# Kernel tuning notes

Hardware: AMD Instinct MI355X
Metric: run time of the kernel (lower is better)

Reference implementation:

```python
import jax, jax.numpy as jnp
import numpy as np

EPS = 1e-5
DIL = 1
PAD = 1
STRIDE = 1

def conv2d(x, w, stride=1, pad=1, dil=1):
    return jax.lax.conv_general_dilated(x, w, (stride, stride), [(pad, pad), (pad, pad)],
                                        rhs_dilation=(dil, dil),
                                        dimension_numbers=('NCHW', 'OIHW', 'NCHW'))

def batchnorm(x, g, b, m, v):
    inv = g / jnp.sqrt(v + EPS)
    return x * inv[None, :, None, None] + (b - m * inv)[None, :, None, None]

def _bilinear(img, y, x):
    # img: [C,H,W]; y,x: [Ho,Wo] float sample coords; zero padding outside.
    H, W = img.shape[1], img.shape[2]
    y0 = jnp.floor(y); x0 = jnp.floor(x)
    ty = y - y0; tx = x - x0
    y0i = y0.astype(jnp.int32); x0i = x0.astype(jnp.int32)
    def g(yi, xi):
        valid = (yi >= 0) & (yi < H) & (xi >= 0) & (xi < W)
        v = img[:, jnp.clip(yi, 0, H - 1), jnp.clip(xi, 0, W - 1)]  # [C,Ho,Wo]
        return jnp.where(valid[None], v, jnp.zeros((), img.dtype))
    return (g(y0i, x0i) * ((1 - ty) * (1 - tx))[None]
            + g(y0i, x0i + 1) * ((1 - ty) * tx)[None]
            + g(y0i + 1, x0i) * (ty * (1 - tx))[None]
            + g(y0i + 1, x0i + 1) * (ty * tx)[None])

def deform_conv(x, w, offset, stride=1, pad=1, dil=1):
    # offset: [B, 18, Ho, Wo], channels 0:9 = dy per kernel tap (row-major), 9:18 = dx.
    B, C, H, W = x.shape
    Co = w.shape[0]
    Ho = (H + 2 * pad - dil * 2 - 1) // stride + 1
    Wo = (W + 2 * pad - dil * 2 - 1) // stride + 1
    off = offset.reshape(B, 2, 9, Ho, Wo)
    iy = (jnp.arange(Ho) * stride - pad).astype(x.dtype)
    ix = (jnp.arange(Wo) * stride - pad).astype(x.dtype)
    wk = w.reshape(Co, C, 9)
    out = jnp.zeros((B, Co, Ho, Wo), x.dtype)
    for k in range(9):  # fixed 3x3 kernel taps
        ky, kx = k // 3, k % 3
        ys = iy[:, None] + ky * dil + off[:, 0, k]  # [B,Ho,Wo]
        xs = ix[None, :] + kx * dil + off[:, 1, k]
        val = jax.vmap(_bilinear)(x, ys, xs)        # [B,C,Ho,Wo]
        out = out + jnp.einsum('bchw,oc->bohw', val, wk[:, :, k])
    return out

def offset_bias(dil, dtype):
    bw = jnp.array([[-1., 0., 1.]] * 3, dtype) * (dil - 1)
    bh = bw.T
    return jnp.concatenate([bh.reshape(-1), bw.reshape(-1)])  # [18]

def setup_inputs() -> dict:
    key = jax.random.key(0)
    ks = jax.random.split(key, 12)
    B, C, H, W = 8, 256, 56, 56
    inp = {
        'x': jax.random.normal(ks[0], (B, C, H, W), jnp.float32),
        'conv1_w': jax.random.normal(ks[1], (C, C, 3, 3), jnp.float32) * 0.02,
        'bn1_g': jax.random.normal(ks[2], (C,), jnp.float32) * 0.1 + 1.0,
        'bn1_b': jax.random.normal(ks[3], (C,), jnp.float32) * 0.1,
        'bn1_m': jax.random.normal(ks[4], (C,), jnp.float32) * 0.1,
        'bn1_v': jax.random.uniform(ks[5], (C,), jnp.float32) + 0.5,
        'off_w': jax.random.normal(ks[6], (18, C, 3, 3), jnp.float32) * 0.01,
        'off_b': jnp.zeros((18,), jnp.float32),
        'conv2_w': jax.random.normal(ks[7], (C, C, 3, 3), jnp.float32) * 0.02,
        'bn2_g': jax.random.normal(ks[8], (C,), jnp.float32) * 0.1 + 1.0,
        'bn2_b': jax.random.normal(ks[9], (C,), jnp.float32) * 0.1,
        'bn2_m': jax.random.normal(ks[10], (C,), jnp.float32) * 0.1,
        'bn2_v': jax.random.uniform(ks[11], (C,), jnp.float32) + 0.5,
    }
    return inp

def reference(x, conv1_w, bn1_g, bn1_b, bn1_m, bn1_v, off_w, off_b, conv2_w, bn2_g, bn2_b, bn2_m, bn2_v):
    residual = x
    out = conv2d(x, conv1_w, STRIDE, PAD, DIL)
    out = jax.nn.relu(batchnorm(out, bn1_g, bn1_b, bn1_m, bn1_v))
    offset = conv2d(out, off_w, STRIDE, PAD, DIL) + off_b[None, :, None, None]
    offset = offset + offset_bias(DIL, out.dtype)[None, :, None, None]
    out = deform_conv(out, conv2_w, offset, STRIDE, PAD, DIL)
    out = batchnorm(out, bn2_g, bn2_b, bn2_m, bn2_v)
    return jax.nn.relu(out + residual)
```

## Files before the change

kernel.cpp:

```cpp
#include <hip/hip_runtime.h>

#define NB 8
#define NH 56
#define NW 56
#define NHW 3136
#define NCHW 802816
#define NPIX 25088
#define NHP 58
#define EPSV 1e-5f

typedef float f32x4 __attribute__((ext_vector_type(4)));
typedef __bf16 bf16x8 __attribute__((ext_vector_type(8)));

__device__ __forceinline__ unsigned short f2b(float f) {
  unsigned int u = __float_as_uint(f);
  u += 0x7FFFu + ((u >> 16) & 1u);
  return (unsigned short)(u >> 16);
}
__device__ __forceinline__ float blo(unsigned int u){ return __uint_as_float(u << 16); }
__device__ __forceinline__ float bhi(unsigned int u){ return __uint_as_float(u & 0xFFFF0000u); }
__device__ __forceinline__ unsigned int pack_trunc(float f0, float f1) {
  return __builtin_amdgcn_perm(__float_as_uint(f1), __float_as_uint(f0), 0x07060302u);
}
__device__ __forceinline__ void soft_barrier() {
  __builtin_amdgcn_s_waitcnt(0xC07F);
  __builtin_amdgcn_s_barrier();
}

__global__ __launch_bounds__(256) void clear_borders(
    unsigned short* __restrict__ xbp, unsigned short* __restrict__ t1b)
{
  int i = blockIdx.x*256 + threadIdx.x;
  int q = i & 31; int pid = i >> 5;
  int b = pid / 228, j = pid % 228;
  int y, x;
  if (j < 58)       { y = 0;  x = j; }
  else if (j < 116) { y = 57; x = j - 58; }
  else { int jj = j - 116; y = 1 + (jj >> 1); x = (jj & 1) * 57; }
  size_t addr = ((size_t)(b*NHP + y)*NHP + x)*256 + q*8;
  uint4 z = make_uint4(0u,0u,0u,0u);
  *(uint4*)(xbp + addr) = z;
  *(uint4*)(t1b + addr) = z;
}

__global__ __launch_bounds__(256) void prep_x(
    const float* __restrict__ x, unsigned short* __restrict__ xbp)
{
  __shared__ float T[64][65];
  const int pxt  = blockIdx.x * 64;
  const int cg   = blockIdx.y * 64;
  const int b    = pxt / NHW;
  const int rem0 = pxt % NHW;
  const int t    = threadIdx.x;
  const int pl   = t & 63;
  const int c0   = t >> 6;
  const float* src = x + (size_t)b*NCHW + rem0;
  #pragma unroll
  for (int it = 0; it < 16; ++it) {
    int c = c0 + it*4;
    T[c][pl] = src[(size_t)(cg + c)*NHW + pl];
  }
  __syncthreads();
  const int pr = t >> 5;
  const int cp = t & 31;
  #pragma unroll
  for (int it = 0; it < 8; ++it) {
    int pxl = pr + it*8;
    int rem = rem0 + pxl;
    int ho = rem / NW, wo = rem % NW;
    unsigned int pk = ((unsigned int)f2b(T[cp*2+1][pxl]) << 16) | (unsigned int)f2b(T[cp*2][pxl]);
    *(unsigned int*)(xbp + ((size_t)(b*NHP + ho + 1)*NHP + (wo + 1))*256 + cg + cp*2) = pk;
  }
}

__global__ __launch_bounds__(256) void prep_w(
    const float* __restrict__ w, unsigned short* __restrict__ wp)
{
  int i = blockIdx.x*256 + threadIdx.x;
  int co = i / 2304;
  int r  = i % 2304;
  int k  = r >> 8;
  int ci = r & 255;
  wp[i] = f2b(w[((size_t)co*256 + ci)*9 + k]);
}

__global__ __launch_bounds__(256) void prep_w3(
    const float* __restrict__ ow, unsigned short* __restrict__ w3p)
{
  int i = blockIdx.x*256 + threadIdx.x;
  int co = i / 2304;
  int r  = i % 2304;
  int k  = r >> 8;
  int ci = r & 255;
  w3p[i] = (co < 18) ? f2b(ow[((size_t)co*256 + ci)*9 + k]) : (unsigned short)0;
}

__global__ __launch_bounds__(512, 4) void gemm_conv1(
    const unsigned short* __restrict__ xbp, const unsigned short* __restrict__ w1p,
    const float* __restrict__ gam, const float* __restrict__ bet,
    const float* __restrict__ mu,  const float* __restrict__ var,
    unsigned short* __restrict__ t1b)
{
  __shared__ unsigned short SMEM[20480];
  unsigned short* Al = SMEM;
  unsigned short* Bl = SMEM + 4096;

  const int m0   = blockIdx.x * 64;
  const int t    = threadIdx.x;
  const int lane = t & 63;
  const int wv   = t >> 6;
  const int wvM  = wv & 1;
  const int wvN  = wv >> 1;
  const int quad = lane >> 4;
  const int l15  = lane & 15;

  const int srow = t >> 3;
  const int seg  = t & 7;
  const int sxor = srow & 7;
  const int px  = m0 + srow;
  const int b   = px / NHW, rem = px % NHW;
  const int ho  = rem / NW, wo = rem % NW;
  const unsigned int pbase = ((unsigned int)(b*NHP + ho)*NHP + wo)*256u + seg*8u;

  f32x4 acc[2][4];
  #pragma unroll
  for (int i = 0; i < 2; ++i)
    #pragma unroll
    for (int j = 0; j < 4; ++j) acc[i][j] = (f32x4)(0.f);

  uint4 pA, pB0, pB1, pB2, pB3;
  {
    pA  = *(const uint4*)(xbp + pbase);
    const unsigned int rb = seg*8u;
    pB0 = *(const uint4*)(w1p + (size_t)(srow      )*2304 + rb);
    pB1 = *(const uint4*)(w1p + (size_t)(srow +  64)*2304 + rb);
    pB2 = *(const uint4*)(w1p + (size_t)(srow + 128)*2304 + rb);
    pB3 = *(const uint4*)(w1p + (size_t)(srow + 192)*2304 + rb);
  }

  for (int r = 0; r < 36; ++r) {
    __syncthreads();
    *(uint4*)(&Al[srow*64 + ((seg ^ sxor)*8)]) = pA;
    *(uint4*)(&Bl[(srow      )*64 + ((seg ^ sxor)*8)]) = pB0;
    *(uint4*)(&Bl[(srow +  64)*64 + ((seg ^ sxor)*8)]) = pB1;
    *(uint4*)(&Bl[(srow + 128)*64 + ((seg ^ sxor)*8)]) = pB2;
    *(uint4*)(&Bl[(srow + 192)*64 + ((seg ^ sxor)*8)]) = pB3;
    {
      const int rn = (r < 35) ? r + 1 : 35;
      const int kn = rn >> 2, cicn = rn & 3;
      const int kyn = kn/3, kxn = kn - kyn*3;
      pA  = *(const uint4*)(xbp + pbase + (unsigned int)((kyn*NHP + kxn)*256 + cicn*64));
      const unsigned int rb = (unsigned int)(rn*64) + seg*8u;
      pB0 = *(const uint4*)(w1p + (size_t)(srow      )*2304 + rb);
      pB1 = *(const uint4*)(w1p + (size_t)(srow +  64)*2304 + rb);
      pB2 = *(const uint4*)(w1p + (size_t)(srow + 128)*2304 + rb);
      pB3 = *(const uint4*)(w1p + (size_t)(srow + 192)*2304 + rb);
    }
    soft_barrier();
    #pragma unroll
    for (int kk = 0; kk < 2; ++kk) {
      const int s8 = (kk*4 + quad) ^ (l15 & 7);
      bf16x8 af[2], bfr[4];
      #pragma unroll
      for (int mt = 0; mt < 2; ++mt)
        af[mt] = *(const bf16x8*)(&Al[(wvM*32 + mt*16 + l15)*64 + s8*8]);
      #pragma unroll
      for (int nt = 0; nt < 4; ++nt)
        bfr[nt] = *(const bf16x8*)(&Bl[(wvN*64 + nt*16 + l15)*64 + s8*8]);
      #pragma unroll
      for (int mt = 0; mt < 2; ++mt)
        #pragma unroll
        for (int nt = 0; nt < 4; ++nt)
          acc[mt][nt] = __builtin_amdgcn_mfma_f32_16x16x32_bf16(af[mt], bfr[nt], acc[mt][nt], 0, 0, 0);
    }
  }

  __syncthreads();
  unsigned short* Sw = SMEM + wv*2304;
  #pragma unroll
  for (int nt = 0; nt < 4; ++nt) {
    const int co = wvN*64 + nt*16 + l15;
    const float inv  = gam[co] * rsqrtf(var[co] + EPSV);
    const float beta = bet[co] - mu[co]*inv;
    #pragma unroll
    for (int mt = 0; mt < 2; ++mt) {
      #pragma unroll
      for (int rr = 0; rr < 4; ++rr) {
        const int pxl = mt*16 + quad*4 + rr;
        float val = acc[mt][nt][rr]*inv + beta;
        val = val > 0.f ? val : 0.f;
        Sw[pxl*72 + nt*16 + l15] = f2b(val);
      }
    }
  }
  #pragma unroll
  for (int i = 0; i < 4; ++i) {
    const int pxl = (lane >> 3) + 8*i;
    const int sc  = lane & 7;
    uint4 q = *(const uint4*)(&Sw[pxl*72 + sc*8]);
    const int pg = m0 + wvM*32 + pxl;
    const int bb = pg / NHW, rm = pg % NHW;
    const int hh = rm / NW, ww = rm % NW;
    *(uint4*)(t1b + ((size_t)(bb*NHP + hh + 1)*NHP + ww + 1)*256 + wvN*64 + sc*8) = q;
  }
}

__global__ __launch_bounds__(256, 8) void gemm_off(
    const unsigned short* __restrict__ t1b, const unsigned short* __restrict__ w3p,
    const float* __restrict__ ob, float* __restrict__ toff)
{
  __shared__ unsigned short Al[4096];
  __shared__ unsigned short Bl[2048];

  const int m0 = blockIdx.x * 64;
  const int kc = blockIdx.y;
  const int t    = threadIdx.x;
  const int lane = t & 63;
  const int wv   = t >> 6;
  const int quad = lane >> 4;
  const int l15  = lane & 15;

  const int arow = t >> 2;
  const int as4  = t & 3;
  const int axor = arow & 7;
  const int pxa  = m0 + arow;
  const int ba   = pxa / NHW, rema = pxa % NHW;
  const unsigned int pbase = ((unsigned int)(ba*NHP + rema/NW)*NHP + rema%NW)*256u;

  const int brow = t >> 3;
  const int bs   = t & 7;

  f32x4 acc[2];
  #pragma unroll
  for (int nt = 0; nt < 2; ++nt) {
    float init = 0.f;
    if (kc == 0) { int co = nt*16 + l15; init = (co < 18) ? ob[co] : 0.f; }
    acc[nt] = (f32x4)(init);
  }

  uint4 pA0, pA1, pB;
  {
    const int r = kc*9, k = r >> 2, cic = r & 3;
    const int ky = k/3, kx = k - ky*3;
    const unsigned int base = pbase + (unsigned int)((ky*NHP + kx)*256 + cic*64);
    pA0 = *(const uint4*)(t1b + base + as4*8);
    pA1 = *(const uint4*)(t1b + base + (as4+4)*8);
    pB  = *(const uint4*)(w3p + (size_t)brow*2304 + r*64 + bs*8);
  }

  for (int rr = 0; rr < 9; ++rr) {
    const int r = kc*9 + rr;
    __syncthreads();
    *(uint4*)(&Al[arow*64 + ((as4     ^ axor)*8)]) = pA0;
    *(uint4*)(&Al[arow*64 + (((as4+4) ^ axor)*8)]) = pA1;
    *(uint4*)(&Bl[brow*64 + ((bs ^ (brow & 7))*8)]) = pB;
    {
      const int rn = (rr < 8) ? r + 1 : r;
      const int kn = rn >> 2, cicn = rn & 3;
      const int kyn = kn/3, kxn = kn - kyn*3;
      const unsigned int base = pbase + (unsigned int)((kyn*NHP + kxn)*256 + cicn*64);
      pA0 = *(const uint4*)(t1b + base + as4*8);
      pA1 = *(const uint4*)(t1b + base + (as4+4)*8);
      pB  = *(const uint4*)(w3p + (size_t)brow*2304 + rn*64 + bs*8);
    }
    soft_barrier();
    #pragma unroll
    for (int kk = 0; kk < 2; ++kk) {
      const int s8 = (kk*4 + quad) ^ (l15 & 7);
      bf16x8 af = *(const bf16x8*)(&Al[(wv*16 + l15)*64 + s8*8]);
      #pragma unroll
      for (int nt = 0; nt < 2; ++nt) {
        bf16x8 bfr = *(const bf16x8*)(&Bl[(nt*16 + l15)*64 + s8*8]);
        acc[nt] = __builtin_amdgcn_mfma_f32_16x16x32_bf16(af, bfr, acc[nt], 0, 0, 0);
      }
    }
  }
  #pragma unroll
  for (int nt = 0; nt < 2; ++nt) {
    const int co = nt*16 + l15;
    if (co < 18) {
      #pragma unroll
      for (int rr2 = 0; rr2 < 4; ++rr2) {
        const int pg = m0 + wv*16 + quad*4 + rr2;
        const int bb = pg / NHW, rm = pg % NHW;
        atomicAdd(&toff[(size_t)bb*(18*NHW) + (size_t)co*NHW + rm], acc[nt][rr2]);
      }
    }
  }
}

__global__ __launch_bounds__(512, 4) void gemm_deform(
    const unsigned short* __restrict__ t1b, const unsigned short* __restrict__ w2p,
    const float* __restrict__ toff, const float* __restrict__ xres,
    const float* __restrict__ gam, const float* __restrict__ bet,
    const float* __restrict__ mu,  const float* __restrict__ var,
    float* __restrict__ outp)
{
  __shared__ unsigned short SMEM[20480];
  unsigned short* Al = SMEM;
  unsigned short* Bl = SMEM + 4096;

  const int m0   = blockIdx.x * 64;
  const int t    = threadIdx.x;
  const int lane = t & 63;
  const int wv   = t >> 6;
  const int wvM  = wv & 1;
  const int wvN  = wv >> 1;
  const int quad = lane >> 4;
  const int l15  = lane & 15;

  const int srow = t >> 3;
  const int seg  = t & 7;
  const int sxor = srow & 7;
  const int px   = m0 + srow;
  const int b    = px / NHW, rem = px % NHW;
  const int ho   = rem / NW, wo = rem % NW;
  const int obb  = b*(18*NHW) + rem;
  const unsigned int prowb = (unsigned int)(b*NHP);

  f32x4 acc[2][4];
  #pragma unroll
  for (int i = 0; i < 2; ++i)
    #pragma unroll
    for (int j = 0; j < 4; ++j) acc[i][j] = (f32x4)(0.f);

  unsigned int o00, o01, o10, o11;
  float w00, w01, w10, w11;
#define COORDS(KK) {                                                   \
    const int ky_ = (KK)/3, kx_ = (KK) - ky_*3;                        \
    const float offy = toff[obb + (KK)*NHW];                           \
    const float offx = toff[obb + (9+(KK))*NHW];                       \
    const float yf = (float)(ho - 1 + ky_) + offy;                     \
    const float xf = (float)(wo - 1 + kx_) + offx;                     \
    const float y0f = floorf(yf), x0f = floorf(xf);                    \
    const float ty = yf - y0f,   tx = xf - x0f;                        \
    const int y0p = (int)y0f + 1, x0p = (int)x0f + 1;                  \
    const int cy0 = min(max(y0p,   0), NHP-1);                         \
    const int cy1 = min(max(y0p+1, 0), NHP-1);                         \
    const int cx0 = min(max(x0p,   0), NHP-1);                         \
    const int cx1 = min(max(x0p+1, 0), NHP-1);                         \
    w00 = (1.f-ty)*(1.f-tx);  w01 = (1.f-ty)*tx;                       \
    w10 = ty*(1.f-tx);        w11 = ty*tx;                             \
    o00 = ((prowb + cy0)*NHP + cx0)*256u + seg*8u;                     \
    o01 = ((prowb + cy0)*NHP + cx1)*256u + seg*8u;                     \
    o10 = ((prowb + cy1)*NHP + cx0)*256u + seg*8u;                     \
    o11 = ((prowb + cy1)*NHP + cx1)*256u + seg*8u;                     \
  }

  COORDS(0);
  uint4 pc00, pc01, pc10, pc11, pB0, pB1, pB2, pB3;
  {
    pc00 = *(const uint4*)(t1b + o00);
    pc01 = *(const uint4*)(t1b + o01);
    pc10 = *(const uint4*)(t1b + o10);
    pc11 = *(const uint4*)(t1b + o11);
    const unsigned int rb = seg*8u;
    pB0 = *(const uint4*)(w2p + (size_t)(srow      )*2304 + rb);
    pB1 = *(const uint4*)(w2p + (size_t)(srow +  64)*2304 + rb);
    pB2 = *(const uint4*)(w2p + (size_t)(srow + 128)*2304 + rb);
    pB3 = *(const uint4*)(w2p + (size_t)(srow + 192)*2304 + rb);
  }

  for (int r = 0; r < 36; ++r) {
    __syncthreads();
    {
      uint4 res;
      {
        float a0 = w00*blo(pc00.x) + w01*blo(pc01.x) + w10*blo(pc10.x) + w11*blo(pc11.x);
        float a1 = w00*bhi(pc00.x) + w01*bhi(pc01.x) + w10*bhi(pc10.x) + w11*bhi(pc11.x);
        res.x = pack_trunc(a0, a1);
      }
      {
        float a0 = w00*blo(pc00.y) + w01*blo(pc01.y) + w10*blo(pc10.y) + w11*blo(pc11.y);
        float a1 = w00*bhi(pc00.y) + w01*bhi(pc01.y) + w10*bhi(pc10.y) + w11*bhi(pc11.y);
        res.y = pack_trunc(a0, a1);
      }
      {
        float a0 = w00*blo(pc00.z) + w01*blo(pc01.z) + w10*blo(pc10.z) + w11*blo(pc11.z);
        float a1 = w00*bhi(pc00.z) + w01*bhi(pc01.z) + w10*bhi(pc10.z) + w11*bhi(pc11.z);
        res.z = pack_trunc(a0, a1);
      }
      {
        float a0 = w00*blo(pc00.w) + w01*blo(pc01.w) + w10*blo(pc10.w) + w11*blo(pc11.w);
        float a1 = w00*bhi(pc00.w) + w01*bhi(pc01.w) + w10*bhi(pc10.w) + w11*bhi(pc11.w);
        res.w = pack_trunc(a0, a1);
      }
      *(uint4*)(&Al[srow*64 + ((seg ^ sxor)*8)]) = res;
    }
    *(uint4*)(&Bl[(srow      )*64 + ((seg ^ sxor)*8)]) = pB0;
    *(uint4*)(&Bl[(srow +  64)*64 + ((seg ^ sxor)*8)]) = pB1;
    *(uint4*)(&Bl[(srow + 128)*64 + ((seg ^ sxor)*8)]) = pB2;
    *(uint4*)(&Bl[(srow + 192)*64 + ((seg ^ sxor)*8)]) = pB3;
    {
      if ((r & 3) == 3 && r < 35) COORDS((r+1) >> 2);
      const int rn = (r < 35) ? r + 1 : 35;
      const unsigned int cio = (unsigned int)((rn & 3)*64);
      pc00 = *(const uint4*)(t1b + o00 + cio);
      pc01 = *(const uint4*)(t1b + o01 + cio);
      pc10 = *(const uint4*)(t1b + o10 + cio);
      pc11 = *(const uint4*)(t1b + o11 + cio);
      const unsigned int rb = (unsigned int)(rn*64) + seg*8u;
      pB0 = *(const uint4*)(w2p + (size_t)(srow      )*2304 + rb);
      pB1 = *(const uint4*)(w2p + (size_t)(srow +  64)*2304 + rb);
      pB2 = *(const uint4*)(w2p + (size_t)(srow + 128)*2304 + rb);
      pB3 = *(const uint4*)(w2p + (size_t)(srow + 192)*2304 + rb);
    }
    soft_barrier();
    #pragma unroll
    for (int kk = 0; kk < 2; ++kk) {
      const int s8 = (kk*4 + quad) ^ (l15 & 7);
      bf16x8 af[2], bfr[4];
      #pragma unroll
      for (int mt = 0; mt < 2; ++mt)
        af[mt] = *(const bf16x8*)(&Al[(wvM*32 + mt*16 + l15)*64 + s8*8]);
      #pragma unroll
      for (int nt = 0; nt < 4; ++nt)
        bfr[nt] = *(const bf16x8*)(&Bl[(wvN*64 + nt*16 + l15)*64 + s8*8]);
      #pragma unroll
      for (int mt = 0; mt < 2; ++mt)
        #pragma unroll
        for (int nt = 0; nt < 4; ++nt)
          acc[mt][nt] = __builtin_amdgcn_mfma_f32_16x16x32_bf16(af[mt], bfr[nt], acc[mt][nt], 0, 0, 0);
    }
  }
#undef COORDS

  __syncthreads();
  float* Sl = (float*)SMEM + wv*1056;
  const int pxl_r = lane & 31;
  const int csel  = lane >> 5;
  const int pg    = m0 + wvM*32 + pxl_r;
  const int bo    = pg / NHW, remo = pg % NHW;
  const size_t obase = (size_t)bo*NCHW + remo;
  #pragma unroll
  for (int h = 0; h < 2; ++h) {
    #pragma unroll
    for (int nt2 = 0; nt2 < 2; ++nt2) {
      const int nt = h*2 + nt2;
      #pragma unroll
      for (int mt = 0; mt < 2; ++mt) {
        #pragma unroll
        for (int rr = 0; rr < 4; ++rr) {
          const int pxl = mt*16 + quad*4 + rr;
          Sl[pxl*33 + nt2*16 + l15] = acc[mt][nt][rr];
        }
      }
    }
    #pragma unroll
    for (int j = 0; j < 16; ++j) {
      const int col = csel*16 + j;
      const int co  = wvN*64 + h*32 + col;
      const float inv  = gam[co] * rsqrtf(var[co] + EPSV);
      const float beta = bet[co] - mu[co]*inv;
      const size_t off = obase + (size_t)co*NHW;
      float val = Sl[pxl_r*33 + col];
      float o = val*inv + beta + xres[off];
      outp[off] = o > 0.f ? o : 0.f;
    }
  }
}

extern "C" void kernel_launch(void* const* d_in, const int* in_sizes, int n_in,
                              void* d_out, int out_size, void* d_ws, size_t ws_size,
                              hipStream_t stream) {
  const float* x   = (const float*)d_in[0];
  const float* w1  = (const float*)d_in[1];
  const float* g1  = (const float*)d_in[2];
  const float* b1  = (const float*)d_in[3];
  const float* m1  = (const float*)d_in[4];
  const float* v1  = (const float*)d_in[5];
  const float* ow  = (const float*)d_in[6];
  const float* ob  = (const float*)d_in[7];
  const float* w2  = (const float*)d_in[8];
  const float* g2  = (const float*)d_in[9];
  const float* b2  = (const float*)d_in[10];
  const float* m2  = (const float*)d_in[11];
  const float* v2  = (const float*)d_in[12];
  float* out = (float*)d_out;

  const size_t PADSZ = (size_t)NB*NHP*NHP*256;
  unsigned short* xbp = (unsigned short*)d_ws;
  unsigned short* t1b = xbp + PADSZ;
  float*          tof = (float*)(t1b + PADSZ);
  unsigned short* w1p = (unsigned short*)(tof + (size_t)NB*18*NHW);
  unsigned short* w2p = w1p + (size_t)589824;
  unsigned short* w3p = w2p + (size_t)589824;

  clear_borders<<<228, 256, 0, stream>>>(xbp, t1b);
  dim3 gp(392, 4, 1);
  prep_x<<<gp, 256, 0, stream>>>(x, xbp);
  prep_w<<<2304, 256, 0, stream>>>(w1, w1p);
  prep_w<<<2304, 256, 0, stream>>>(w2, w2p);
  prep_w3<<<288, 256, 0, stream>>>(ow, w3p);
  hipMemsetAsync(tof, 0, (size_t)NB*18*NHW*sizeof(float), stream);

  gemm_conv1<<<392, 512, 0, stream>>>(xbp, w1p, g1, b1, m1, v1, t1b);
  dim3 go(392, 4, 1);
  gemm_off<<<go, 256, 0, stream>>>(t1b, w3p, ob, tof);
  gemm_deform<<<392, 512, 0, stream>>>(t1b, w2p, tof, x, g2, b2, m2, v2, out);
}
```

Measured before the change: 255.6 us.

## Load weight fragments directly from global in MFMA layout; double-buffer A tile

Weights are repacked into a fragment-major layout so each lane loads its MFMA B operand straight from global memory into registers, bypassing LDS for B in all three GEMM kernels. The A tile in LDS becomes double-buffered with one barrier per K step, and global loads for the next step are issued in half-steps between MFMA groups using sched barriers. This cuts LDS traffic and barrier count, but adds register pressure and relies on L2/L1 hits for weight reuse across blocks.

```diff
diff --git a/kernel.cpp b/kernel.cpp
--- a/kernel.cpp
+++ b/kernel.cpp
@@ -22,10 +22,7 @@
 __device__ __forceinline__ unsigned int pack_trunc(float f0, float f1) {
   return __builtin_amdgcn_perm(__float_as_uint(f1), __float_as_uint(f0), 0x07060302u);
 }
-__device__ __forceinline__ void soft_barrier() {
-  __builtin_amdgcn_s_waitcnt(0xC07F);
-  __builtin_amdgcn_s_barrier();
-}
+__device__ __forceinline__ bf16x8 asbf(const uint4& q) { return *(const bf16x8*)&q; }
 
 __global__ __launch_bounds__(256) void clear_borders(
     unsigned short* __restrict__ xbp, unsigned short* __restrict__ t1b)
@@ -73,37 +70,46 @@
   }
 }
 
-__global__ __launch_bounds__(256) void prep_w(
-    const float* __restrict__ w, unsigned short* __restrict__ wp)
+__global__ __launch_bounds__(256) void prep_wq(
+    const float* __restrict__ w, unsigned short* __restrict__ wq)
 {
   int i = blockIdx.x*256 + threadIdx.x;
-  int co = i / 2304;
-  int r  = i % 2304;
-  int k  = r >> 8;
-  int ci = r & 255;
-  wp[i] = f2b(w[((size_t)co*256 + ci)*9 + k]);
-}
-
-__global__ __launch_bounds__(256) void prep_w3(
-    const float* __restrict__ ow, unsigned short* __restrict__ w3p)
+  int j  = i & 7;
+  int n  = (i >> 3) & 255;
+  int kc = (i >> 11) & 7;
+  int r  = i >> 14;
+  int ktap = r >> 2, cic = r & 3;
+  int ci = cic*64 + kc*8 + j;
+  wq[i] = f2b(w[((size_t)n*256 + ci)*9 + ktap]);
+}
+
+__global__ __launch_bounds__(256) void prep_wq3(
+    const float* __restrict__ ow, unsigned short* __restrict__ wq)
 {
   int i = blockIdx.x*256 + threadIdx.x;
-  int co = i / 2304;
-  int r  = i % 2304;
-  int k  = r >> 8;
-  int ci = r & 255;
-  w3p[i] = (co < 18) ? f2b(ow[((size_t)co*256 + ci)*9 + k]) : (unsigned short)0;
+  int j  = i & 7;
+  int n  = (i >> 3) & 31;
+  int kc = (i >> 8) & 7;
+  int r  = i >> 11;
+  int ktap = r >> 2, cic = r & 3;
+  int ci = cic*64 + kc*8 + j;
+  wq[i] = (n < 18) ? f2b(ow[((size_t)n*256 + ci)*9 + ktap]) : (unsigned short)0;
+}
+
+__device__ __forceinline__ int tapoff(int r) {
+  int k = r >> 2, cic = r & 3;
+  int ky = k/3, kx = k - ky*3;
+  return (ky*NHP + kx)*256 + cic*64;
 }
 
 __global__ __launch_bounds__(512, 4) void gemm_conv1(
-    const unsigned short* __restrict__ xbp, const unsigned short* __restrict__ w1p,
+    const unsigned short* __restrict__ xbp, const unsigned short* __restrict__ w1q,
     const float* __restrict__ gam, const float* __restrict__ bet,
     const float* __restrict__ mu,  const float* __restrict__ var,
     unsigned short* __restrict__ t1b)
 {
-  __shared__ unsigned short SMEM[20480];
+  __shared__ unsigned short SMEM[18432];
   unsigned short* Al = SMEM;
-  unsigned short* Bl = SMEM + 4096;
 
   const int m0   = blockIdx.x * 64;
   const int t    = threadIdx.x;
@@ -114,68 +120,69 @@
   const int quad = lane >> 4;
   const int l15  = lane & 15;
 
-  const int srow = t >> 3;
-  const int seg  = t & 7;
-  const int sxor = srow & 7;
-  const int px  = m0 + srow;
-  const int b   = px / NHW, rem = px % NHW;
-  const int ho  = rem / NW, wo = rem % NW;
+  const int srow = t >> 3, seg = t & 7, sxor = srow & 7;
+  const int px = m0 + srow;
+  const int b = px / NHW, rem = px % NHW;
+  const int ho = rem / NW, wo = rem % NW;
   const unsigned int pbase = ((unsigned int)(b*NHP + ho)*NHP + wo)*256u + seg*8u;
 
+  const unsigned short* bqb = w1q + (size_t)(wvN*64 + l15)*8;
+#define BQ1(R,KK,NT) (const uint4*)(bqb + ((size_t)(((R)*8 + (KK)*4 + quad))*256 + (NT)*16)*8)
+
   f32x4 acc[2][4];
   #pragma unroll
   for (int i = 0; i < 2; ++i)
     #pragma unroll
     for (int j = 0; j < 4; ++j) acc[i][j] = (f32x4)(0.f);
 
-  uint4 pA, pB0, pB1, pB2, pB3;
+  uint4 pb0[4];
   {
-    pA  = *(const uint4*)(xbp + pbase);
-    const unsigned int rb = seg*8u;
-    pB0 = *(const uint4*)(w1p + (size_t)(srow      )*2304 + rb);
-    pB1 = *(const uint4*)(w1p + (size_t)(srow +  64)*2304 + rb);
-    pB2 = *(const uint4*)(w1p + (size_t)(srow + 128)*2304 + rb);
-    pB3 = *(const uint4*)(w1p + (size_t)(srow + 192)*2304 + rb);
+    uint4 pA = *(const uint4*)(xbp + pbase + tapoff(0));
+    #pragma unroll
+    for (int nt = 0; nt < 4; ++nt) pb0[nt] = *BQ1(0,0,nt);
+    *(uint4*)(&Al[srow*64 + ((seg ^ sxor)*8)]) = pA;
+    __syncthreads();
   }
 
   for (int r = 0; r < 36; ++r) {
-    __syncthreads();
-    *(uint4*)(&Al[srow*64 + ((seg ^ sxor)*8)]) = pA;
-    *(uint4*)(&Bl[(srow      )*64 + ((seg ^ sxor)*8)]) = pB0;
-    *(uint4*)(&Bl[(srow +  64)*64 + ((seg ^ sxor)*8)]) = pB1;
-    *(uint4*)(&Bl[(srow + 128)*64 + ((seg ^ sxor)*8)]) = pB2;
-    *(uint4*)(&Bl[(srow + 192)*64 + ((seg ^ sxor)*8)]) = pB3;
-    {
-      const int rn = (r < 35) ? r + 1 : 35;
-      const int kn = rn >> 2, cicn = rn & 3;
-      const int kyn = kn/3, kxn = kn - kyn*3;
-      pA  = *(const uint4*)(xbp + pbase + (unsigned int)((kyn*NHP + kxn)*256 + cicn*64));
-      const unsigned int rb = (unsigned int)(rn*64) + seg*8u;
-      pB0 = *(const uint4*)(w1p + (size_t)(srow      )*2304 + rb);
-      pB1 = *(const uint4*)(w1p + (size_t)(srow +  64)*2304 + rb);
-      pB2 = *(const uint4*)(w1p + (size_t)(srow + 128)*2304 + rb);
-      pB3 = *(const uint4*)(w1p + (size_t)(srow + 192)*2304 + rb);
-    }
-    soft_barrier();
-    #pragma unroll
-    for (int kk = 0; kk < 2; ++kk) {
-      const int s8 = (kk*4 + quad) ^ (l15 & 7);
-      bf16x8 af[2], bfr[4];
-      #pragma unroll
-      for (int mt = 0; mt < 2; ++mt)
-        af[mt] = *(const bf16x8*)(&Al[(wvM*32 + mt*16 + l15)*64 + s8*8]);
-      #pragma unroll
-      for (int nt = 0; nt < 4; ++nt)
-        bfr[nt] = *(const bf16x8*)(&Bl[(wvN*64 + nt*16 + l15)*64 + s8*8]);
-      #pragma unroll
-      for (int mt = 0; mt < 2; ++mt)
-        #pragma unroll
-        for (int nt = 0; nt < 4; ++nt)
-          acc[mt][nt] = __builtin_amdgcn_mfma_f32_16x16x32_bf16(af[mt], bfr[nt], acc[mt][nt], 0, 0, 0);
-    }
-  }
-
-  __syncthreads();
+    const int cur = (r & 1) * 4096;
+    const int nxt = 4096 - cur;
+    const int rn  = (r < 35) ? r + 1 : 35;
+    uint4 pAn = *(const uint4*)(xbp + pbase + tapoff(rn));
+    uint4 pb1[4];
+    #pragma unroll
+    for (int nt = 0; nt < 4; ++nt) pb1[nt] = *BQ1(r,1,nt);
+    __builtin_amdgcn_sched_barrier(0);
+    {
+      const int s8 = quad ^ (l15 & 7);
+      bf16x8 af0 = *(const bf16x8*)(&Al[cur + (wvM*32 +      l15)*64 + s8*8]);
+      bf16x8 af1 = *(const bf16x8*)(&Al[cur + (wvM*32 + 16 + l15)*64 + s8*8]);
+      #pragma unroll
+      for (int nt = 0; nt < 4; ++nt) {
+        bf16x8 bv = asbf(pb0[nt]);
+        acc[0][nt] = __builtin_amdgcn_mfma_f32_16x16x32_bf16(af0, bv, acc[0][nt], 0, 0, 0);
+        acc[1][nt] = __builtin_amdgcn_mfma_f32_16x16x32_bf16(af1, bv, acc[1][nt], 0, 0, 0);
+      }
+    }
+    #pragma unroll
+    for (int nt = 0; nt < 4; ++nt) pb0[nt] = *BQ1(rn,0,nt);
+    __builtin_amdgcn_sched_barrier(0);
+    {
+      const int s8 = (4 + quad) ^ (l15 & 7);
+      bf16x8 af0 = *(const bf16x8*)(&Al[cur + (wvM*32 +      l15)*64 + s8*8]);
+      bf16x8 af1 = *(const bf16x8*)(&Al[cur + (wvM*32 + 16 + l15)*64 + s8*8]);
+      #pragma unroll
+      for (int nt = 0; nt < 4; ++nt) {
+        bf16x8 bv = asbf(pb1[nt]);
+        acc[0][nt] = __builtin_amdgcn_mfma_f32_16x16x32_bf16(af0, bv, acc[0][nt], 0, 0, 0);
+        acc[1][nt] = __builtin_amdgcn_mfma_f32_16x16x32_bf16(af1, bv, acc[1][nt], 0, 0, 0);
+      }
+    }
+    *(uint4*)(&Al[nxt + srow*64 + ((seg ^ sxor)*8)]) = pAn;
+    __syncthreads();
+  }
+#undef BQ1
+
   unsigned short* Sw = SMEM + wv*2304;
   #pragma unroll
   for (int nt = 0; nt < 4; ++nt) {
@@ -193,6 +200,8 @@
       }
     }
   }
+  __builtin_amdgcn_s_waitcnt(0xC07F);
+  __builtin_amdgcn_s_barrier();
   #pragma unroll
   for (int i = 0; i < 4; ++i) {
     const int pxl = (lane >> 3) + 8*i;
@@ -205,12 +214,11 @@
   }
 }
 
-__global__ __launch_bounds__(256, 8) void gemm_off(
-    const unsigned short* __restrict__ t1b, const unsigned short* __restrict__ w3p,
+__global__ __launch_bounds__(256, 6) void gemm_off(
+    const unsigned short* __restrict__ t1b, const unsigned short* __restrict__ w3q,
     const float* __restrict__ ob, float* __restrict__ toff)
 {
-  __shared__ unsigned short Al[4096];
-  __shared__ unsigned short Bl[2048];
+  __shared__ unsigned short Al[2*4096];
 
   const int m0 = blockIdx.x * 64;
   const int kc = blockIdx.y;
@@ -220,15 +228,13 @@
   const int quad = lane >> 4;
   const int l15  = lane & 15;
 
-  const int arow = t >> 2;
-  const int as4  = t & 3;
-  const int axor = arow & 7;
-  const int pxa  = m0 + arow;
-  const int ba   = pxa / NHW, rema = pxa % NHW;
+  const int arow = t >> 2, as4 = t & 3, axor = arow & 7;
+  const int pxa = m0 + arow;
+  const int ba = pxa / NHW, rema = pxa % NHW;
   const unsigned int pbase = ((unsigned int)(ba*NHP + rema/NW)*NHP + rema%NW)*256u;
 
-  const int brow = t >> 3;
-  const int bs   = t & 7;
+  const unsigned short* bqb = w3q + (size_t)l15*8;
+#define BQ3(R,KK,NT) (const uint4*)(bqb + ((size_t)(((R)*8 + (KK)*4 + quad))*32 + (NT)*16)*8)
 
   f32x4 acc[2];
   #pragma unroll
@@ -238,43 +244,52 @@
     acc[nt] = (f32x4)(init);
   }
 
-  uint4 pA0, pA1, pB;
+  uint4 pb0[2];
   {
-    const int r = kc*9, k = r >> 2, cic = r & 3;
-    const int ky = k/3, kx = k - ky*3;
-    const unsigned int base = pbase + (unsigned int)((ky*NHP + kx)*256 + cic*64);
-    pA0 = *(const uint4*)(t1b + base + as4*8);
-    pA1 = *(const uint4*)(t1b + base + (as4+4)*8);
-    pB  = *(const uint4*)(w3p + (size_t)brow*2304 + r*64 + bs*8);
-  }
-
-  for (int rr = 0; rr < 9; ++rr) {
-    const int r = kc*9 + rr;
-    __syncthreads();
+    const int r0 = kc*9;
+    uint4 pA0 = *(const uint4*)(t1b + pbase + tapoff(r0) + as4*8);
+    uint4 pA1 = *(const uint4*)(t1b + pbase + tapoff(r0) + (as4+4)*8);
+    #pragma unroll
+    for (int nt = 0; nt < 2; ++nt) pb0[nt] = *BQ3(r0,0,nt);
     *(uint4*)(&Al[arow*64 + ((as4     ^ axor)*8)]) = pA0;
     *(uint4*)(&Al[arow*64 + (((as4+4) ^ axor)*8)]) = pA1;
-    *(uint4*)(&Bl[brow*64 + ((bs ^ (brow & 7))*8)]) = pB;
-    {
-      const int rn = (rr < 8) ? r + 1 : r;
-      const int kn = rn >> 2, cicn = rn & 3;
-      const int kyn = kn/3, kxn = kn - kyn*3;
-      const unsigned int base = pbase + (unsigned int)((kyn*NHP + kxn)*256 + cicn*64);
-      pA0 = *(const uint4*)(t1b + base + as4*8);
-      pA1 = *(const uint4*)(t1b + base + (as4+4)*8);
-      pB  = *(const uint4*)(w3p + (size_t)brow*2304 + rn*64 + bs*8);
-    }
-    soft_barrier();
-    #pragma unroll
-    for (int kk = 0; kk < 2; ++kk) {
-      const int s8 = (kk*4 + quad) ^ (l15 & 7);
-      bf16x8 af = *(const bf16x8*)(&Al[(wv*16 + l15)*64 + s8*8]);
-      #pragma unroll
-      for (int nt = 0; nt < 2; ++nt) {
-        bf16x8 bfr = *(const bf16x8*)(&Bl[(nt*16 + l15)*64 + s8*8]);
-        acc[nt] = __builtin_amdgcn_mfma_f32_16x16x32_bf16(af, bfr, acc[nt], 0, 0, 0);
-      }
-    }
-  }
+    __syncthreads();
+  }
+
+  for (int rr = 0; rr < 9; ++rr) {
+    const int r   = kc*9 + rr;
+    const int cur = (rr & 1) * 4096;
+    const int nxt = 4096 - cur;
+    const int rn  = (rr < 8) ? r + 1 : r;
+    uint4 pA0 = *(const uint4*)(t1b + pbase + tapoff(rn) + as4*8);
+    uint4 pA1 = *(const uint4*)(t1b + pbase + tapoff(rn) + (as4+4)*8);
+    uint4 pb1[2];
+    #pragma unroll
+    for (int nt = 0; nt < 2; ++nt) pb1[nt] = *BQ3(r,1,nt);
+    __builtin_amdgcn_sched_barrier(0);
+    {
+      const int s8 = quad ^ (l15 & 7);
+      bf16x8 af = *(const bf16x8*)(&Al[cur + (wv*16 + l15)*64 + s8*8]);
+      #pragma unroll
+      for (int nt = 0; nt < 2; ++nt)
+        acc[nt] = __builtin_amdgcn_mfma_f32_16x16x32_bf16(af, asbf(pb0[nt]), acc[nt], 0, 0, 0);
+    }
+    #pragma unroll
+    for (int nt = 0; nt < 2; ++nt) pb0[nt] = *BQ3(rn,0,nt);
+    __builtin_amdgcn_sched_barrier(0);
+    {
+      const int s8 = (4 + quad) ^ (l15 & 7);
+      bf16x8 af = *(const bf16x8*)(&Al[cur + (wv*16 + l15)*64 + s8*8]);
+      #pragma unroll
+      for (int nt = 0; nt < 2; ++nt)
+        acc[nt] = __builtin_amdgcn_mfma_f32_16x16x32_bf16(af, asbf(pb1[nt]), acc[nt], 0, 0, 0);
+    }
+    *(uint4*)(&Al[nxt + arow*64 + ((as4     ^ axor)*8)]) = pA0;
+    *(uint4*)(&Al[nxt + arow*64 + (((as4+4) ^ axor)*8)]) = pA1;
+    __syncthreads();
+  }
+#undef BQ3
+
   #pragma unroll
   for (int nt = 0; nt < 2; ++nt) {
     const int co = nt*16 + l15;
@@ -290,15 +305,14 @@
 }
 
 __global__ __launch_bounds__(512, 4) void gemm_deform(
-    const unsigned short* __restrict__ t1b, const unsigned short* __restrict__ w2p,
+    const unsigned short* __restrict__ t1b, const unsigned short* __restrict__ w2q,
     const float* __restrict__ toff, const float* __restrict__ xres,
     const float* __restrict__ gam, const float* __restrict__ bet,
     const float* __restrict__ mu,  const float* __restrict__ var,
     float* __restrict__ outp)
 {
-  __shared__ unsigned short SMEM[20480];
-  unsigned short* Al = SMEM;
-  unsigned short* Bl = SMEM + 4096;
+  __shared__ float SMEMF[8448];
+  unsigned short* Al = (unsigned short*)SMEMF;
 
   const int m0   = blockIdx.x * 64;
   const int t    = threadIdx.x;
@@ -309,14 +323,15 @@
   const int quad = lane >> 4;
   const int l15  = lane & 15;
 
-  const int srow = t >> 3;
-  const int seg  = t & 7;
-  const int sxor = srow & 7;
-  const int px   = m0 + srow;
-  const int b    = px / NHW, rem = px % NHW;
-  const int ho   = rem / NW, wo = rem % NW;
-  const int obb  = b*(18*NHW) + rem;
+  const int srow = t >> 3, seg = t & 7, sxor = srow & 7;
+  const int px = m0 + srow;
+  const int b = px / NHW, rem = px % NHW;
+  const int ho = rem / NW, wo = rem % NW;
+  const int obb = b*(18*NHW) + rem;
   const unsigned int prowb = (unsigned int)(b*NHP);
+
+  const unsigned short* bqb = w2q + (size_t)(wvN*64 + l15)*8;
+#define BQ2(R,KK,NT) (const uint4*)(bqb + ((size_t)(((R)*8 + (KK)*4 + quad))*256 + (NT)*16)*8)
 
   f32x4 acc[2][4];
   #pragma unroll
@@ -346,87 +361,87 @@
     o10 = ((prowb + cy1)*NHP + cx0)*256u + seg*8u;                     \
     o11 = ((prowb + cy1)*NHP + cx1)*256u + seg*8u;                     \
   }
-
-  COORDS(0);
-  uint4 pc00, pc01, pc10, pc11, pB0, pB1, pB2, pB3;
+#define BILIN(RES, C00, C01, C10, C11) {                                             \
+    uint4 res_;                                                                      \
+    { float a0 = w00*blo(C00.x)+w01*blo(C01.x)+w10*blo(C10.x)+w11*blo(C11.x);        \
+      float a1 = w00*bhi(C00.x)+w01*bhi(C01.x)+w10*bhi(C10.x)+w11*bhi(C11.x);        \
+      res_.x = pack_trunc(a0, a1); }                                                 \
+    { float a0 = w00*blo(C00.y)+w01*blo(C01.y)+w10*blo(C10.y)+w11*blo(C11.y);        \
+      float a1 = w00*bhi(C00.y)+w01*bhi(C01.y)+w10*bhi(C10.y)+w11*bhi(C11.y);        \
+      res_.y = pack_trunc(a0, a1); }                                                 \
+    { float a0 = w00*blo(C00.z)+w01*blo(C01.z)+w10*blo(C10.z)+w11*blo(C11.z);        \
+      float a1 = w00*bhi(C00.z)+w01*bhi(C01.z)+w10*bhi(C10.z)+w11*bhi(C11.z);        \
+      res_.z = pack_trunc(a0, a1); }                                                 \
+    { float a0 = w00*blo(C00.w)+w01*blo(C01.w)+w10*blo(C10.w)+w11*blo(C11.w);        \
+      float a1 = w00*bhi(C00.w)+w01*bhi(C01.w)+w10*bhi(C10.w)+w11*bhi(C11.w);        \
+      res_.w = pack_trunc(a0, a1); }                                                 \
+    RES = res_;                                                                      \
+  }
+
+  uint4 pb0[4];
   {
-    pc00 = *(const uint4*)(t1b + o00);
-    pc01 = *(const uint4*)(t1b + o01);
-    pc10 = *(const uint4*)(t1b + o10);
-    pc11 = *(const uint4*)(t1b + o11);
-    const unsigned int rb = seg*8u;
-    pB0 = *(const uint4*)(w2p + (size_t)(srow      )*2304 + rb);
-    pB1 = *(const uint4*)(w2p + (size_t)(srow +  64)*2304 + rb);
-    pB2 = *(const uint4*)(w2p + (size_t)(srow + 128)*2304 + rb);
-    pB3 = *(const uint4*)(w2p + (size_t)(srow + 192)*2304 + rb);
+    COORDS(0);
+    uint4 c00 = *(const uint4*)(t1b + o00);
+    uint4 c01 = *(const uint4*)(t1b + o01);
+    uint4 c10 = *(const uint4*)(t1b + o10);
+    uint4 c11 = *(const uint4*)(t1b + o11);
+    #pragma unroll
+    for (int nt = 0; nt < 4; ++nt) pb0[nt] = *BQ2(0,0,nt);
+    uint4 res; BILIN(res, c00, c01, c10, c11);
+    *(uint4*)(&Al[srow*64 + ((seg ^ sxor)*8)]) = res;
+    __syncthreads();
   }
 
   for (int r = 0; r < 36; ++r) {
-    __syncthreads();
-    {
-      uint4 res;
-      {
-        float a0 = w00*blo(pc00.x) + w01*blo(pc01.x) + w10*blo(pc10.x) + w11*blo(pc11.x);
-        float a1 = w00*bhi(pc00.x) + w01*bhi(pc01.x) + w10*bhi(pc10.x) + w11*bhi(pc11.x);
-        res.x = pack_trunc(a0, a1);
-      }
-      {
-        float a0 = w00*blo(pc00.y) + w01*blo(pc01.y) + w10*blo(pc10.y) + w11*blo(pc11.y);
-        float a1 = w00*bhi(pc00.y) + w01*bhi(pc01.y) + w10*bhi(pc10.y) + w11*bhi(pc11.y);
-        res.y = pack_trunc(a0, a1);
-      }
-      {
-        float a0 = w00*blo(pc00.z) + w01*blo(pc01.z) + w10*blo(pc10.z) + w11*blo(pc11.z);
-        float a1 = w00*bhi(pc00.z) + w01*bhi(pc01.z) + w10*bhi(pc10.z) + w11*bhi(pc11.z);
-        res.z = pack_trunc(a0, a1);
-      }
-      {
-        float a0 = w00*blo(pc00.w) + w01*blo(pc01.w) + w10*blo(pc10.w) + w11*blo(pc11.w);
-        float a1 = w00*bhi(pc00.w) + w01*bhi(pc01.w) + w10*bhi(pc10.w) + w11*bhi(pc11.w);
-        res.w = pack_trunc(a0, a1);
-      }
-      *(uint4*)(&Al[srow*64 + ((seg ^ sxor)*8)]) = res;
-    }
-    *(uint4*)(&Bl[(srow      )*64 + ((seg ^ sxor)*8)]) = pB0;
-    *(uint4*)(&Bl[(srow +  64)*64 + ((seg ^ sxor)*8)]) = pB1;
-    *(uint4*)(&Bl[(srow + 128)*64 + ((seg ^ sxor)*8)]) = pB2;
-    *(uint4*)(&Bl[(srow + 192)*64 + ((seg ^ sxor)*8)]) = pB3;
-    {
-      if ((r & 3) == 3 && r < 35) COORDS((r+1) >> 2);
-      const int rn = (r < 35) ? r + 1 : 35;
-      const unsigned int cio = (unsigned int)((rn & 3)*64);
-      pc00 = *(const uint4*)(t1b + o00 + cio);
-      pc01 = *(const uint4*)(t1b + o01 + cio);
-      pc10 = *(const uint4*)(t1b + o10 + cio);
-      pc11 = *(const uint4*)(t1b + o11 + cio);
-      const unsigned int rb = (unsigned int)(rn*64) + seg*8u;
-      pB0 = *(const uint4*)(w2p + (size_t)(srow      )*2304 + rb);
-      pB1 = *(const uint4*)(w2p + (size_t)(srow +  64)*2304 + rb);
-      pB2 = *(const uint4*)(w2p + (size_t)(srow + 128)*2304 + rb);
-      pB3 = *(const uint4*)(w2p + (size_t)(srow + 192)*2304 + rb);
-    }
-    soft_barrier();
-    #pragma unroll
-    for (int kk = 0; kk < 2; ++kk) {
-      const int s8 = (kk*4 + quad) ^ (l15 & 7);
-      bf16x8 af[2], bfr[4];
-      #pragma unroll
-      for (int mt = 0; mt < 2; ++mt)
-        af[mt] = *(const bf16x8*)(&Al[(wvM*32 + mt*16 + l15)*64 + s8*8]);
-      #pragma unroll
-      for (int nt = 0; nt < 4; ++nt)
-        bfr[nt] = *(const bf16x8*)(&Bl[(wvN*64 + nt*16 + l15)*64 + s8*8]);
-      #pragma unroll
-      for (int mt = 0; mt < 2; ++mt)
-        #pragma unroll
-        for (int nt = 0; nt < 4; ++nt)
-          acc[mt][nt] = __builtin_amdgcn_mfma_f32_16x16x32_bf16(af[mt], bfr[nt], acc[mt][nt], 0, 0, 0);
-    }
-  }
+    const int cur = (r & 1) * 4096;
+    const int nxt = 4096 - cur;
+    const int rn  = (r < 35) ? r + 1 : 35;
+    if ((r & 3) == 3 && r < 35) COORDS((r+1) >> 2);
+    const unsigned int cioN = (unsigned int)((rn & 3)*64);
+    uint4 c00 = *(const uint4*)(t1b + o00 + cioN);
+    uint4 c01 = *(const uint4*)(t1b + o01 + cioN);
+    uint4 c10 = *(const uint4*)(t1b + o10 + cioN);
+    uint4 c11 = *(const uint4*)(t1b + o11 + cioN);
+    uint4 pb1[4];
+    #pragma unroll
+    for (int nt = 0; nt < 4; ++nt) pb1[nt] = *BQ2(r,1,nt);
+    __builtin_amdgcn_sched_barrier(0);
+    {
+      const int s8 = quad ^ (l15 & 7);
+      bf16x8 af0 = *(const bf16x8*)(&Al[cur + (wvM*32 +      l15)*64 + s8*8]);
+      bf16x8 af1 = *(const bf16x8*)(&Al[cur + (wvM*32 + 16 + l15)*64 + s8*8]);
+      #pragma unroll
+      for (int nt = 0; nt < 4; ++nt) {
+        bf16x8 bv = asbf(pb0[nt]);
+        acc[0][nt] = __builtin_amdgcn_mfma_f32_16x16x32_bf16(af0, bv, acc[0][nt], 0, 0, 0);
+        acc[1][nt] = __builtin_amdgcn_mfma_f32_16x16x32_bf16(af1, bv, acc[1][nt], 0, 0, 0);
+      }
+    }
+    #pragma unroll
+    for (int nt = 0; nt < 4; ++nt) pb0[nt] = *BQ2(rn,0,nt);
+    __builtin_amdgcn_sched_barrier(0);
+    {
+      const int s8 = (4 + quad) ^ (l15 & 7);
+      bf16x8 af0 = *(const bf16x8*)(&Al[cur + (wvM*32 +      l15)*64 + s8*8]);
+      bf16x8 af1 = *(const bf16x8*)(&Al[cur + (wvM*32 + 16 + l15)*64 + s8*8]);
+      #pragma unroll
+      for (int nt = 0; nt < 4; ++nt) {
+        bf16x8 bv = asbf(pb1[nt]);
+        acc[0][nt] = __builtin_amdgcn_mfma_f32_16x16x32_bf16(af0, bv, acc[0][nt], 0, 0, 0);
+        acc[1][nt] = __builtin_amdgcn_mfma_f32_16x16x32_bf16(af1, bv, acc[1][nt], 0, 0, 0);
+      }
+    }
+    {
+      uint4 res; BILIN(res, c00, c01, c10, c11);
+      *(uint4*)(&Al[nxt + srow*64 + ((seg ^ sxor)*8)]) = res;
+    }
+    __syncthreads();
+  }
+#undef BQ2
 #undef COORDS
-
-  __syncthreads();
-  float* Sl = (float*)SMEM + wv*1056;
+#undef BILIN
+
+  float* Sl = SMEMF + wv*1056;
   const int pxl_r = lane & 31;
   const int csel  = lane >> 5;
   const int pg    = m0 + wvM*32 + pxl_r;
@@ -434,6 +449,7 @@
   const size_t obase = (size_t)bo*NCHW + remo;
   #pragma unroll
   for (int h = 0; h < 2; ++h) {
+    __syncthreads();
     #pragma unroll
     for (int nt2 = 0; nt2 < 2; ++nt2) {
       const int nt = h*2 + nt2;
@@ -446,6 +462,8 @@
         }
       }
     }
+    __builtin_amdgcn_s_waitcnt(0xC07F);
+    __builtin_amdgcn_s_barrier();
     #pragma unroll
     for (int j = 0; j < 16; ++j) {
       const int col = csel*16 + j;
@@ -482,20 +500,20 @@
   unsigned short* xbp = (unsigned short*)d_ws;
   unsigned short* t1b = xbp + PADSZ;
   float*          tof = (float*)(t1b + PADSZ);
-  unsigned short* w1p = (unsigned short*)(tof + (size_t)NB*18*NHW);
-  unsigned short* w2p = w1p + (size_t)589824;
-  unsigned short* w3p = w2p + (size_t)589824;
+  unsigned short* w1q = (unsigned short*)(tof + (size_t)NB*18*NHW);
+  unsigned short* w2q = w1q + (size_t)589824;
+  unsigned short* w3q = w2q + (size_t)589824;
 
   clear_borders<<<228, 256, 0, stream>>>(xbp, t1b);
   dim3 gp(392, 4, 1);
   prep_x<<<gp, 256, 0, stream>>>(x, xbp);
-  prep_w<<<2304, 256, 0, stream>>>(w1, w1p);
-  prep_w<<<2304, 256, 0, stream>>>(w2, w2p);
-  prep_w3<<<288, 256, 0, stream>>>(ow, w3p);
+  prep_wq<<<2304, 256, 0, stream>>>(w1, w1q);
+  prep_wq<<<2304, 256, 0, stream>>>(w2, w2q);
+  prep_wq3<<<288, 256, 0, stream>>>(ow, w3q);
   hipMemsetAsync(tof, 0, (size_t)NB*18*NHW*sizeof(float), stream);
 
-  gemm_conv1<<<392, 512, 0, stream>>>(xbp, w1p, g1, b1, m1, v1, t1b);
+  gemm_conv1<<<392, 512, 0, stream>>>(xbp, w1q, g1, b1, m1, v1, t1b);
   dim3 go(392, 4, 1);
-  gemm_off<<<go, 256, 0, stream>>>(t1b, w3p, ob, tof);
-  gemm_deform<<<392, 512, 0, stream>>>(t1b, w2p, tof, x, g2, b2, m2, v2, out);
-}
+  gemm_off<<<go, 256, 0, stream>>>(t1b, w3q, ob, tof);
+  gemm_deform<<<392, 512, 0, stream>>>(t1b, w2q, tof, x, g2, b2, m2, v2, out);
+}
```

New measurement: 264.3 us. 3.4% more time.
